# Optimization experiments

Measured on AMD Instinct MI355X. Metric: run time of the kernel, lower is better.

## Reference

```python
import jax, jax.numpy as jnp
import numpy as np

B, L, D, N, KEEP, HID = 64, 256, 128, 8192, 64, 1024
IN_DIM = D + KEEP * D + 1  # q + packed subset keys + log_count


def setup_inputs() -> dict:
    key = jax.random.key(0)
    ks = jax.random.split(key, 7)
    q = jax.random.normal(ks[0], (N, D), jnp.float32)
    k = jax.random.normal(ks[1], (B, L, D), jnp.float32)
    batch_idx = jax.random.randint(ks[2], (N,), 0, B)
    mask = jax.random.randint(ks[3], (N, L), 0, 2).astype(bool)
    count = jax.random.randint(ks[4], (N,), 0, L)
    W1 = jax.random.normal(ks[5], (IN_DIM, HID), jnp.float32) / np.sqrt(IN_DIM).astype(np.float32)
    b1 = jnp.zeros((HID,), jnp.float32)
    W2 = jax.random.normal(ks[6], (HID, 1), jnp.float32) / np.sqrt(HID).astype(np.float32)
    b2 = jnp.zeros((1,), jnp.float32)
    return dict(q=q, k=k, batch_idx=batch_idx, mask=mask, count=count,
                W1=W1, b1=b1, W2=W2, b2=b2)


def _pack_subset_keys(k, batch_idx, mask):
    # chain_k: [N, L, D] gather of per-chain key blocks
    chain_k = k[batch_idx]
    pos = jnp.arange(L, dtype=jnp.float32)
    # score = L - pos for masked positions, 0 otherwise -> topk picks first KEEP masked positions
    scores = mask.astype(jnp.float32) * (jnp.float32(L) - pos)[None, :]
    top_scores, top_idx = jax.lax.top_k(scores, KEEP)
    picked = top_scores > 0
    sortable = jnp.where(picked, top_idx, L)  # sentinel L for unpicked
    sortable = jnp.sort(sortable, axis=1)     # restore ascending position order
    picked = sortable < L
    safe_idx = jnp.where(picked, sortable, 0)
    packed = jnp.take_along_axis(chain_k, safe_idx[:, :, None], axis=1)  # [N, KEEP, D]
    packed = packed * picked[:, :, None].astype(packed.dtype)
    return packed.reshape(N, KEEP * D)


def reference(q, k, batch_idx, mask, count, W1, b1, W2, b2):
    packed = _pack_subset_keys(k, batch_idx, mask)
    log_count = jnp.log1p(count.astype(q.dtype))[:, None]
    feat = jnp.concatenate([q, packed, log_count], axis=-1)  # [N, IN_DIM]
    h = jax.nn.gelu(feat @ W1 + b1, approximate=False)       # torch GELU = exact erf
    return (h @ W2 + b2).squeeze(-1)                          # [N]
```

## Files before the change

### kernel.cpp

```cpp
#include <hip/hip_runtime.h>
#include <math.h>

#define N_ROWS 8192
#define B_CH   64
#define L_SEQ  256
#define D_DIM  128
#define KEEP   64
#define HID    1024
#define KTOT   8320

#define KOFF   (N_ROWS * D_DIM)
#define ZOFF   (KOFF + B_CH * L_SEQ * D_DIM)
#define BUF_ELEMS (ZOFF + 128)

#define QK_BLOCKS   1537
#define W1T_BLOCKS  2080
#define PACK_BLOCKS 64
#define OUT_BLOCKS  32
#define PREP_GRID   (QK_BLOCKS + W1T_BLOCKS + PACK_BLOCKS + OUT_BLOCKS)

typedef unsigned short ushort_t;
typedef __attribute__((ext_vector_type(8))) short  short8;
typedef __attribute__((ext_vector_type(4))) float  float4v;


__device__ __forceinline__ ushort_t f2bf(float f) {
    union { float f; unsigned int u; } v; v.f = f;
    unsigned int u = v.u;
    unsigned int r = u + 0x7fffu + ((u >> 16) & 1u);
    return (ushort_t)(r >> 16);
}

__device__ __forceinline__ void glds16(const void* g, void* l) {
    __builtin_amdgcn_global_load_lds(
        (const __attribute__((address_space(1))) unsigned int*)g,
        (__attribute__((address_space(3))) unsigned int*)l,
        16, 0, 0);
}

__global__ void prep(const float* __restrict__ q, const float* __restrict__ k,
                     const float* __restrict__ W1, const int* __restrict__ mask,
                     const int* __restrict__ batch_idx, const int* __restrict__ count,
                     const float* __restrict__ b2,
                     ushort_t* __restrict__ buf, ushort_t* __restrict__ w1t,
                     int* __restrict__ srcLUT, float* __restrict__ logc,
                     float* __restrict__ out) {
    __shared__ __align__(16) char smem[34304];
    const int blk = blockIdx.x;
    const int t = threadIdx.x;

    if (blk < QK_BLOCKS) {
        int c = blk * 256 + t;
        if (c >= BUF_ELEMS / 8) return;
        int e = c * 8;
        float4 x0, x1;
        if (e < KOFF) {
            const float4* s = (const float4*)(q + e);
            x0 = s[0]; x1 = s[1];
        } else if (e < ZOFF) {
            const float4* s = (const float4*)(k + (e - KOFF));
            x0 = s[0]; x1 = s[1];
        } else {
            x0 = make_float4(0.f, 0.f, 0.f, 0.f);
            x1 = x0;
        }
        union { ushort_t s[8]; uint4 v; } o;
        o.s[0] = f2bf(x0.x); o.s[1] = f2bf(x0.y); o.s[2] = f2bf(x0.z); o.s[3] = f2bf(x0.w);
        o.s[4] = f2bf(x1.x); o.s[5] = f2bf(x1.y); o.s[6] = f2bf(x1.z); o.s[7] = f2bf(x1.w);
        *(uint4*)(buf + e) = o.v;

    } else if (blk < QK_BLOCKS + W1T_BLOCKS) {
        const int idx = blk - QK_BLOCKS;
        const int k0 = (idx % 130) * 64, h0 = (idx / 130) * 64;
        float (*tile)[65] = (float(*)[65])smem;
        const int hl = t & 63, kl = t >> 6;
#pragma unroll
        for (int i = 0; i < 16; ++i) {
            int kk = kl + i * 4;
            tile[kk][hl] = W1[(size_t)(k0 + kk) * HID + h0 + hl];
        }
        __syncthreads();
#pragma unroll
        for (int i = 0; i < 2; ++i) {
            int chunk = i * 256 + t;
            int h = chunk >> 3, piece = chunk & 7;
            union { ushort_t s[8]; uint4 v; } o;
#pragma unroll
            for (int j = 0; j < 8; ++j) o.s[j] = f2bf(tile[piece * 8 + j][h]);
            *(uint4*)(w1t + (size_t)(h0 + h) * KTOT + k0 + piece * 8) = o.v;
        }

    } else if (blk < QK_BLOCKS + W1T_BLOCKS + PACK_BLOCKS) {
        const int p = blk - (QK_BLOCKS + W1T_BLOCKS);
        const int n0 = p * 128;
        int* sidx = (int*)smem;
        int* bidx_l = (int*)(smem + 33280);
        for (int i = t; i < 128 * 65; i += 256) sidx[i] = -1;
        if (t < 128) {
            int n = n0 + t;
            bidx_l[t] = batch_idx[n];
            logc[n] = log1pf((float)count[n]);
            srcLUT[n] = n * D_DIM;
        }
        __syncthreads();
        const int w = t >> 6, l = t & 63;
        const unsigned long long ltm = (1ull << l) - 1ull;
        for (int r = 0; r < 32; ++r) {
            const int lr = w * 32 + r;
            const int n = n0 + lr;
            const int* mrow = mask + (size_t)n * L_SEQ;
            int m0 = mrow[l] != 0;
            int m1 = mrow[64 + l] != 0;
            int m2 = mrow[128 + l] != 0;
            int m3 = mrow[192 + l] != 0;
            unsigned long long b0 = __ballot(m0), b1 = __ballot(m1);
            unsigned long long b2v = __ballot(m2), b3 = __ballot(m3);
            int p1 = (int)__popcll(b0);
            int p2 = p1 + (int)__popcll(b1);
            int p3 = p2 + (int)__popcll(b2v);
            int* row = sidx + lr * 65;
            if (m0) { int rk = (int)__popcll(b0 & ltm);      if (rk < KEEP) row[rk] = l; }
            if (m1) { int rk = p1 + (int)__popcll(b1 & ltm); if (rk < KEEP) row[rk] = 64 + l; }
            if (m2) { int rk = p2 + (int)__popcll(b2v & ltm); if (rk < KEEP) row[rk] = 128 + l; }
            if (m3) { int rk = p3 + (int)__popcll(b3 & ltm); if (rk < KEEP) row[rk] = 192 + l; }
        }
        __syncthreads();
        for (int e = t; e < KEEP * 128; e += 256) {
            int j = e >> 7, nl = e & 127;
            int s = sidx[nl * 65 + j];
            srcLUT[(size_t)(j + 1) * N_ROWS + n0 + nl] =
                (s >= 0) ? (KOFF + (bidx_l[nl] * L_SEQ + s) * D_DIM) : ZOFF;
        }

    } else {
        int i = (blk - (QK_BLOCKS + W1T_BLOCKS + PACK_BLOCKS)) * 256 + t;
        if (i < N_ROWS) out[i] = b2[0];
    }
}

__global__ __launch_bounds__(256, 2)
void gemm_mlp(const ushort_t* __restrict__ buf, const ushort_t* __restrict__ w1t,
              const int* __restrict__ srcLUT, const float* __restrict__ logc,
              const float* __restrict__ W1, const float* __restrict__ b1,
              const float* __restrict__ W2, float* __restrict__ out) {
    __shared__ ushort_t As[128 * 128];
    __shared__ ushort_t Bs[128 * 128];

    const int t = threadIdx.x;
    const int blkH = blockIdx.x, blkM = blockIdx.y;
    const int wave = t >> 6, lane = t & 63;
    const int wm = wave >> 1, wh = wave & 1;
    const int ln = lane & 15, quad = lane >> 4;

    float4v acc[4][4];
#pragma unroll
    for (int i = 0; i < 4; ++i)
#pragma unroll
        for (int j = 0; j < 4; ++j)
#pragma unroll
            for (int r = 0; r < 4; ++r) acc[i][j][r] = 0.0f;

    const int tr = t >> 4;
    const int slot = t & 15;
    const int pg = slot ^ tr;
    ushort_t* lA = As + t * 8;
    ushort_t* lB = Bs + t * 8;
    const ushort_t* gB[8];
#pragma unroll
    for (int i = 0; i < 8; ++i)
        gB[i] = w1t + (size_t)(blkH * 128 + i * 16 + tr) * KTOT + pg * 8;
    const int* lutBase = srcLUT + blkM * 128 + tr;

    int offA[8];
#pragma unroll
    for (int i = 0; i < 8; ++i) offA[i] = lutBase[i * 16];

    for (int bi = 0; bi < 65; ++bi) {
#pragma unroll
        for (int i = 0; i < 8; ++i) {
            glds16(buf + offA[i] + pg * 8, lA + i * 2048);
            glds16(gB[i] + bi * 128, lB + i * 2048);
        }
        int offN[8];
        if (bi < 64) {
#pragma unroll
            for (int i = 0; i < 8; ++i) offN[i] = lutBase[(bi + 1) * N_ROWS + i * 16];
        }
        __syncthreads();
#pragma unroll
        for (int kk = 0; kk < 4; ++kk) {
            short8 af[4], bfr[4];
#pragma unroll
            for (int mi = 0; mi < 4; ++mi) {
                const int row = wm * 64 + mi * 16 + ln;
                const int sl = (kk * 4 + quad) ^ ln;
                af[mi] = *(const short8*)(As + row * 128 + sl * 8);
            }
#pragma unroll
            for (int ni = 0; ni < 4; ++ni) {
                const int row = wh * 64 + ni * 16 + ln;
                const int sl = (kk * 4 + quad) ^ ln;
                bfr[ni] = *(const short8*)(Bs + row * 128 + sl * 8);
            }
#pragma unroll
            for (int mi = 0; mi < 4; ++mi)
#pragma unroll
                for (int ni = 0; ni < 4; ++ni)
                    acc[mi][ni] = __builtin_amdgcn_mfma_f32_16x16x32_bf16(
                        af[mi], bfr[ni], acc[mi][ni], 0, 0, 0);
        }
        __syncthreads();
#pragma unroll
        for (int i = 0; i < 8; ++i) offA[i] = offN[i];
    }

    const float* w1last = W1 + (size_t)KTOT * HID;
    float w1l[4], b1v[4], w2v[4];
#pragma unroll
    for (int ni = 0; ni < 4; ++ni) {
        int h = blkH * 128 + wh * 64 + ni * 16 + ln;
        w1l[ni] = w1last[h];
        b1v[ni] = b1[h];
        w2v[ni] = W2[h];
    }
    const int nbase = blkM * 128 + wm * 64 + quad * 4;
#pragma unroll
    for (int mi = 0; mi < 4; ++mi) {
#pragma unroll
        for (int rg = 0; rg < 4; ++rg) {
            const int n = nbase + mi * 16 + rg;
            const float lc = logc[n];
            float s = 0.0f;
#pragma unroll
            for (int ni = 0; ni < 4; ++ni) {
                float pre = acc[mi][ni][rg] + lc * w1l[ni] + b1v[ni];
                float hv = 0.5f * pre * (1.0f + erff(pre * 0.70710678118654752f));
                s += hv * w2v[ni];
            }
            s += __shfl_xor(s, 1);
            s += __shfl_xor(s, 2);
            s += __shfl_xor(s, 4);
            s += __shfl_xor(s, 8);
            if (ln == 0) atomicAdd(out + n, s);
        }
    }
}

extern "C" void kernel_launch(void* const* d_in, const int* in_sizes, int n_in,
                              void* d_out, int out_size, void* d_ws, size_t ws_size,
                              hipStream_t stream) {
    const float* q     = (const float*)d_in[0];
    const float* k     = (const float*)d_in[1];
    const int*   bidx  = (const int*)d_in[2];
    const int*   mask  = (const int*)d_in[3];
    const int*   count = (const int*)d_in[4];
    const float* W1    = (const float*)d_in[5];
    const float* b1    = (const float*)d_in[6];
    const float* W2    = (const float*)d_in[7];
    const float* b2    = (const float*)d_in[8];
    float* out = (float*)d_out;

    char* ws = (char*)d_ws;
    ushort_t* buf    = (ushort_t*)(ws);
    ushort_t* w1t    = (ushort_t*)(ws + 6291712);
    int*      srcLUT = (int*)(ws + 6291712 + 17039360);
    float*    logc   = (float*)(ws + 6291712 + 17039360 + 2129920);

    prep<<<PREP_GRID, 256, 0, stream>>>(q, k, W1, mask, bidx, count, b2,
                                        buf, w1t, srcLUT, logc, out);
    gemm_mlp<<<dim3(HID / 128, N_ROWS / 128), 256, 0, stream>>>(
        buf, w1t, srcLUT, logc, W1, b1, W2, out);
}
```

Before: 268.7 us.

## Double-buffer GEMM K-chunks in LDS and move finer-grained pack blocks first

The MLP GEMM now splits each 128-wide K block into two 64-wide chunks held in double-buffered LDS. The next chunk's global-to-LDS loads are issued before the MFMAs on the current chunk, leaving one barrier per chunk instead of two per block. LDS use per block also halves. In the prep kernel, mask packing uses 256 smaller blocks of 32 rows, scheduled first, so the serial ballot loop is shorter and overlaps with the conversion blocks. The cost is more loop iterations and some extra index bookkeeping for the LUT offsets across half-blocks.

```diff
diff --git a/kernel.cpp b/kernel.cpp
--- a/kernel.cpp
+++ b/kernel.cpp
@@ -13,16 +13,15 @@
 #define ZOFF   (KOFF + B_CH * L_SEQ * D_DIM)
 #define BUF_ELEMS (ZOFF + 128)
 
+#define PACK_BLOCKS 256
 #define QK_BLOCKS   1537
 #define W1T_BLOCKS  2080
-#define PACK_BLOCKS 64
 #define OUT_BLOCKS  32
-#define PREP_GRID   (QK_BLOCKS + W1T_BLOCKS + PACK_BLOCKS + OUT_BLOCKS)
+#define PREP_GRID   (PACK_BLOCKS + QK_BLOCKS + W1T_BLOCKS + OUT_BLOCKS)
 
 typedef unsigned short ushort_t;
 typedef __attribute__((ext_vector_type(8))) short  short8;
 typedef __attribute__((ext_vector_type(4))) float  float4v;
-
 
 __device__ __forceinline__ ushort_t f2bf(float f) {
     union { float f; unsigned int u; } v; v.f = f;
@@ -45,12 +44,52 @@
                      ushort_t* __restrict__ buf, ushort_t* __restrict__ w1t,
                      int* __restrict__ srcLUT, float* __restrict__ logc,
                      float* __restrict__ out) {
-    __shared__ __align__(16) char smem[34304];
+    __shared__ __align__(16) char smem[16640];
     const int blk = blockIdx.x;
     const int t = threadIdx.x;
 
-    if (blk < QK_BLOCKS) {
-        int c = blk * 256 + t;
+    if (blk < PACK_BLOCKS) {
+        const int n0 = blk * 32;
+        int* sidx = (int*)smem;
+        int* bidx_l = (int*)(smem + 32 * 65 * 4);
+        for (int i = t; i < 32 * 65; i += 256) sidx[i] = -1;
+        if (t < 32) {
+            int n = n0 + t;
+            bidx_l[t] = batch_idx[n];
+            logc[n] = log1pf((float)count[n]);
+            srcLUT[n] = n * D_DIM;
+        }
+        __syncthreads();
+        const int w = t >> 6, l = t & 63;
+        const unsigned long long ltm = (1ull << l) - 1ull;
+        for (int r = 0; r < 8; ++r) {
+            const int lr = w * 8 + r;
+            const int* mrow = mask + (size_t)(n0 + lr) * L_SEQ;
+            int m0 = mrow[l] != 0;
+            int m1 = mrow[64 + l] != 0;
+            int m2 = mrow[128 + l] != 0;
+            int m3 = mrow[192 + l] != 0;
+            unsigned long long b0 = __ballot(m0), b1 = __ballot(m1);
+            unsigned long long b2v = __ballot(m2), b3 = __ballot(m3);
+            int p1 = (int)__popcll(b0);
+            int p2 = p1 + (int)__popcll(b1);
+            int p3 = p2 + (int)__popcll(b2v);
+            int* row = sidx + lr * 65;
+            if (m0) { int rk = (int)__popcll(b0 & ltm);       if (rk < KEEP) row[rk] = l; }
+            if (m1) { int rk = p1 + (int)__popcll(b1 & ltm);  if (rk < KEEP) row[rk] = 64 + l; }
+            if (m2) { int rk = p2 + (int)__popcll(b2v & ltm); if (rk < KEEP) row[rk] = 128 + l; }
+            if (m3) { int rk = p3 + (int)__popcll(b3 & ltm);  if (rk < KEEP) row[rk] = 192 + l; }
+        }
+        __syncthreads();
+        for (int e = t; e < KEEP * 32; e += 256) {
+            int j = e >> 5, nl = e & 31;
+            int s = sidx[nl * 65 + j];
+            srcLUT[(size_t)(j + 1) * N_ROWS + n0 + nl] =
+                (s >= 0) ? (KOFF + (bidx_l[nl] * L_SEQ + s) * D_DIM) : ZOFF;
+        }
+
+    } else if (blk < PACK_BLOCKS + QK_BLOCKS) {
+        int c = (blk - PACK_BLOCKS) * 256 + t;
         if (c >= BUF_ELEMS / 8) return;
         int e = c * 8;
         float4 x0, x1;
@@ -69,8 +108,8 @@
         o.s[4] = f2bf(x1.x); o.s[5] = f2bf(x1.y); o.s[6] = f2bf(x1.z); o.s[7] = f2bf(x1.w);
         *(uint4*)(buf + e) = o.v;
 
-    } else if (blk < QK_BLOCKS + W1T_BLOCKS) {
-        const int idx = blk - QK_BLOCKS;
+    } else if (blk < PACK_BLOCKS + QK_BLOCKS + W1T_BLOCKS) {
+        const int idx = blk - (PACK_BLOCKS + QK_BLOCKS);
         const int k0 = (idx % 130) * 64, h0 = (idx / 130) * 64;
         float (*tile)[65] = (float(*)[65])smem;
         const int hl = t & 63, kl = t >> 6;
@@ -90,50 +129,8 @@
             *(uint4*)(w1t + (size_t)(h0 + h) * KTOT + k0 + piece * 8) = o.v;
         }
 
-    } else if (blk < QK_BLOCKS + W1T_BLOCKS + PACK_BLOCKS) {
-        const int p = blk - (QK_BLOCKS + W1T_BLOCKS);
-        const int n0 = p * 128;
-        int* sidx = (int*)smem;
-        int* bidx_l = (int*)(smem + 33280);
-        for (int i = t; i < 128 * 65; i += 256) sidx[i] = -1;
-        if (t < 128) {
-            int n = n0 + t;
-            bidx_l[t] = batch_idx[n];
-            logc[n] = log1pf((float)count[n]);
-            srcLUT[n] = n * D_DIM;
-        }
-        __syncthreads();
-        const int w = t >> 6, l = t & 63;
-        const unsigned long long ltm = (1ull << l) - 1ull;
-        for (int r = 0; r < 32; ++r) {
-            const int lr = w * 32 + r;
-            const int n = n0 + lr;
-            const int* mrow = mask + (size_t)n * L_SEQ;
-            int m0 = mrow[l] != 0;
-            int m1 = mrow[64 + l] != 0;
-            int m2 = mrow[128 + l] != 0;
-            int m3 = mrow[192 + l] != 0;
-            unsigned long long b0 = __ballot(m0), b1 = __ballot(m1);
-            unsigned long long b2v = __ballot(m2), b3 = __ballot(m3);
-            int p1 = (int)__popcll(b0);
-            int p2 = p1 + (int)__popcll(b1);
-            int p3 = p2 + (int)__popcll(b2v);
-            int* row = sidx + lr * 65;
-            if (m0) { int rk = (int)__popcll(b0 & ltm);      if (rk < KEEP) row[rk] = l; }
-            if (m1) { int rk = p1 + (int)__popcll(b1 & ltm); if (rk < KEEP) row[rk] = 64 + l; }
-            if (m2) { int rk = p2 + (int)__popcll(b2v & ltm); if (rk < KEEP) row[rk] = 128 + l; }
-            if (m3) { int rk = p3 + (int)__popcll(b3 & ltm); if (rk < KEEP) row[rk] = 192 + l; }
-        }
-        __syncthreads();
-        for (int e = t; e < KEEP * 128; e += 256) {
-            int j = e >> 7, nl = e & 127;
-            int s = sidx[nl * 65 + j];
-            srcLUT[(size_t)(j + 1) * N_ROWS + n0 + nl] =
-                (s >= 0) ? (KOFF + (bidx_l[nl] * L_SEQ + s) * D_DIM) : ZOFF;
-        }
-
     } else {
-        int i = (blk - (QK_BLOCKS + W1T_BLOCKS + PACK_BLOCKS)) * 256 + t;
+        int i = (blk - (PACK_BLOCKS + QK_BLOCKS + W1T_BLOCKS)) * 256 + t;
         if (i < N_ROWS) out[i] = b2[0];
     }
 }
@@ -143,8 +140,8 @@
               const int* __restrict__ srcLUT, const float* __restrict__ logc,
               const float* __restrict__ W1, const float* __restrict__ b1,
               const float* __restrict__ W2, float* __restrict__ out) {
-    __shared__ ushort_t As[128 * 128];
-    __shared__ ushort_t Bs[128 * 128];
+    __shared__ ushort_t As[2][128 * 64];
+    __shared__ ushort_t Bs[2][128 * 64];
 
     const int t = threadIdx.x;
     const int blkH = blockIdx.x, blkM = blockIdx.y;
@@ -160,47 +157,59 @@
 #pragma unroll
             for (int r = 0; r < 4; ++r) acc[i][j][r] = 0.0f;
 
-    const int tr = t >> 4;
-    const int slot = t & 15;
-    const int pg = slot ^ tr;
-    ushort_t* lA = As + t * 8;
-    ushort_t* lB = Bs + t * 8;
-    const ushort_t* gB[8];
-#pragma unroll
-    for (int i = 0; i < 8; ++i)
-        gB[i] = w1t + (size_t)(blkH * 128 + i * 16 + tr) * KTOT + pg * 8;
+    const int tr = t >> 3;
+    const int pg = (t & 7) ^ (tr & 7);
+    const ushort_t* gBp[4];
+#pragma unroll
+    for (int i = 0; i < 4; ++i)
+        gBp[i] = w1t + (size_t)(blkH * 128 + i * 32 + tr) * KTOT + pg * 8;
     const int* lutBase = srcLUT + blkM * 128 + tr;
 
-    int offA[8];
-#pragma unroll
-    for (int i = 0; i < 8; ++i) offA[i] = lutBase[i * 16];
-
-    for (int bi = 0; bi < 65; ++bi) {
-#pragma unroll
-        for (int i = 0; i < 8; ++i) {
-            glds16(buf + offA[i] + pg * 8, lA + i * 2048);
-            glds16(gB[i] + bi * 128, lB + i * 2048);
-        }
-        int offN[8];
-        if (bi < 64) {
-#pragma unroll
-            for (int i = 0; i < 8; ++i) offN[i] = lutBase[(bi + 1) * N_ROWS + i * 16];
-        }
-        __syncthreads();
-#pragma unroll
-        for (int kk = 0; kk < 4; ++kk) {
+    int offA[4], offN[4];
+#pragma unroll
+    for (int i = 0; i < 4; ++i) offA[i] = lutBase[i * 32];
+
+#pragma unroll
+    for (int i = 0; i < 4; ++i) {
+        glds16(buf + offA[i] + pg * 8, &As[0][(i * 256 + t) * 8]);
+        glds16(gBp[i], &Bs[0][(i * 256 + t) * 8]);
+    }
+
+    int p = 0;
+    for (int ch = 0; ch < 130; ++ch) {
+        __syncthreads();
+        const int nx = ch + 1;
+        if (nx < 130) {
+            const int half = nx & 1;
+            const int* offs = half ? offA : offN;
+            ushort_t* dA = &As[p ^ 1][0];
+            ushort_t* dB = &Bs[p ^ 1][0];
+#pragma unroll
+            for (int i = 0; i < 4; ++i) {
+                glds16(buf + offs[i] + half * 64 + pg * 8, dA + (i * 256 + t) * 8);
+                glds16(gBp[i] + nx * 64, dB + (i * 256 + t) * 8);
+            }
+        }
+        if ((ch & 1) == 0 && (ch >> 1) < 64) {
+#pragma unroll
+            for (int i = 0; i < 4; ++i) offN[i] = lutBase[((ch >> 1) + 1) * N_ROWS + i * 32];
+        }
+        const ushort_t* rA = &As[p][0];
+        const ushort_t* rB = &Bs[p][0];
+#pragma unroll
+        for (int kk = 0; kk < 2; ++kk) {
             short8 af[4], bfr[4];
 #pragma unroll
             for (int mi = 0; mi < 4; ++mi) {
                 const int row = wm * 64 + mi * 16 + ln;
-                const int sl = (kk * 4 + quad) ^ ln;
-                af[mi] = *(const short8*)(As + row * 128 + sl * 8);
+                const int sl = (kk * 4 + quad) ^ (ln & 7);
+                af[mi] = *(const short8*)(rA + row * 64 + sl * 8);
             }
 #pragma unroll
             for (int ni = 0; ni < 4; ++ni) {
                 const int row = wh * 64 + ni * 16 + ln;
-                const int sl = (kk * 4 + quad) ^ ln;
-                bfr[ni] = *(const short8*)(Bs + row * 128 + sl * 8);
+                const int sl = (kk * 4 + quad) ^ (ln & 7);
+                bfr[ni] = *(const short8*)(rB + row * 64 + sl * 8);
             }
 #pragma unroll
             for (int mi = 0; mi < 4; ++mi)
@@ -209,9 +218,11 @@
                     acc[mi][ni] = __builtin_amdgcn_mfma_f32_16x16x32_bf16(
                         af[mi], bfr[ni], acc[mi][ni], 0, 0, 0);
         }
-        __syncthreads();
-#pragma unroll
-        for (int i = 0; i < 8; ++i) offA[i] = offN[i];
+        if (ch & 1) {
+#pragma unroll
+            for (int i = 0; i < 4; ++i) offA[i] = offN[i];
+        }
+        p ^= 1;
     }
 
     const float* w1last = W1 + (size_t)KTOT * HID;
```

Result: faster. 255.6 us (-4.9%).

## Pre-swizzle W1 into MFMA fragment layout and load B directly to registers

Applied to the files above, without the earlier changes.

The W1 transpose in prep now writes bf16 weights in a per-lane MFMA fragment order, so the GEMM loads B operands straight from global memory into registers with coalesced 16-byte loads. This drops the B shared-memory tile, its global-to-LDS copies and its LDS reads, halving LDS use in the GEMM. The pack-subset work is split into more, smaller blocks placed first in the prep grid, and the output init is folded into them. The cost is higher register pressure from 16 short8 B fragments per iteration, and B loads that are no longer shared across the two M-waves.

```diff
diff --git a/kernel.cpp b/kernel.cpp
--- a/kernel.cpp
+++ b/kernel.cpp
@@ -8,21 +8,21 @@
 #define KEEP   64
 #define HID    1024
 #define KTOT   8320
+#define KTILES 260
+#define HTILES 64
 
 #define KOFF   (N_ROWS * D_DIM)
 #define ZOFF   (KOFF + B_CH * L_SEQ * D_DIM)
 #define BUF_ELEMS (ZOFF + 128)
 
+#define PACK_BLOCKS 256
 #define QK_BLOCKS   1537
 #define W1T_BLOCKS  2080
-#define PACK_BLOCKS 64
-#define OUT_BLOCKS  32
-#define PREP_GRID   (QK_BLOCKS + W1T_BLOCKS + PACK_BLOCKS + OUT_BLOCKS)
+#define PREP_GRID   (PACK_BLOCKS + QK_BLOCKS + W1T_BLOCKS)
 
 typedef unsigned short ushort_t;
 typedef __attribute__((ext_vector_type(8))) short  short8;
 typedef __attribute__((ext_vector_type(4))) float  float4v;
-
 
 __device__ __forceinline__ ushort_t f2bf(float f) {
     union { float f; unsigned int u; } v; v.f = f;
@@ -42,15 +42,56 @@
                      const float* __restrict__ W1, const int* __restrict__ mask,
                      const int* __restrict__ batch_idx, const int* __restrict__ count,
                      const float* __restrict__ b2,
-                     ushort_t* __restrict__ buf, ushort_t* __restrict__ w1t,
+                     ushort_t* __restrict__ buf, ushort_t* __restrict__ w1f,
                      int* __restrict__ srcLUT, float* __restrict__ logc,
                      float* __restrict__ out) {
-    __shared__ __align__(16) char smem[34304];
+    __shared__ __align__(16) char smem[16640];
     const int blk = blockIdx.x;
     const int t = threadIdx.x;
 
-    if (blk < QK_BLOCKS) {
-        int c = blk * 256 + t;
+    if (blk < PACK_BLOCKS) {
+        const int n0 = blk * 32;
+        int* sidx = (int*)smem;
+        int* bidx_l = (int*)(smem + 32 * 65 * 4);
+        for (int i = t; i < 32 * 65; i += 256) sidx[i] = -1;
+        if (t < 32) {
+            int n = n0 + t;
+            bidx_l[t] = batch_idx[n];
+            logc[n] = log1pf((float)count[n]);
+            srcLUT[n] = n * D_DIM;
+            out[n] = b2[0];
+        }
+        __syncthreads();
+        const int w = t >> 6, l = t & 63;
+        const unsigned long long ltm = (1ull << l) - 1ull;
+        for (int r = 0; r < 8; ++r) {
+            const int lr = w * 8 + r;
+            const int* mrow = mask + (size_t)(n0 + lr) * L_SEQ;
+            int m0 = mrow[l] != 0;
+            int m1 = mrow[64 + l] != 0;
+            int m2 = mrow[128 + l] != 0;
+            int m3 = mrow[192 + l] != 0;
+            unsigned long long b0 = __ballot(m0), b1 = __ballot(m1);
+            unsigned long long b2v = __ballot(m2), b3 = __ballot(m3);
+            int p1 = (int)__popcll(b0);
+            int p2 = p1 + (int)__popcll(b1);
+            int p3 = p2 + (int)__popcll(b2v);
+            int* row = sidx + lr * 65;
+            if (m0) { int rk = (int)__popcll(b0 & ltm);       if (rk < KEEP) row[rk] = l; }
+            if (m1) { int rk = p1 + (int)__popcll(b1 & ltm);  if (rk < KEEP) row[rk] = 64 + l; }
+            if (m2) { int rk = p2 + (int)__popcll(b2v & ltm); if (rk < KEEP) row[rk] = 128 + l; }
+            if (m3) { int rk = p3 + (int)__popcll(b3 & ltm);  if (rk < KEEP) row[rk] = 192 + l; }
+        }
+        __syncthreads();
+        for (int e = t; e < KEEP * 32; e += 256) {
+            int j = e >> 5, nl = e & 31;
+            int s = sidx[nl * 65 + j];
+            srcLUT[(size_t)(j + 1) * N_ROWS + n0 + nl] =
+                (s >= 0) ? (KOFF + (bidx_l[nl] * L_SEQ + s) * D_DIM) : ZOFF;
+        }
+
+    } else if (blk < PACK_BLOCKS + QK_BLOCKS) {
+        int c = (blk - PACK_BLOCKS) * 256 + t;
         if (c >= BUF_ELEMS / 8) return;
         int e = c * 8;
         float4 x0, x1;
@@ -69,8 +110,8 @@
         o.s[4] = f2bf(x1.x); o.s[5] = f2bf(x1.y); o.s[6] = f2bf(x1.z); o.s[7] = f2bf(x1.w);
         *(uint4*)(buf + e) = o.v;
 
-    } else if (blk < QK_BLOCKS + W1T_BLOCKS) {
-        const int idx = blk - QK_BLOCKS;
+    } else {
+        const int idx = blk - (PACK_BLOCKS + QK_BLOCKS);
         const int k0 = (idx % 130) * 64, h0 = (idx / 130) * 64;
         float (*tile)[65] = (float(*)[65])smem;
         const int hl = t & 63, kl = t >> 6;
@@ -82,69 +123,26 @@
         __syncthreads();
 #pragma unroll
         for (int i = 0; i < 2; ++i) {
-            int chunk = i * 256 + t;
-            int h = chunk >> 3, piece = chunk & 7;
-            union { ushort_t s[8]; uint4 v; } o;
-#pragma unroll
-            for (int j = 0; j < 8; ++j) o.s[j] = f2bf(tile[piece * 8 + j][h]);
-            *(uint4*)(w1t + (size_t)(h0 + h) * KTOT + k0 + piece * 8) = o.v;
-        }
-
-    } else if (blk < QK_BLOCKS + W1T_BLOCKS + PACK_BLOCKS) {
-        const int p = blk - (QK_BLOCKS + W1T_BLOCKS);
-        const int n0 = p * 128;
-        int* sidx = (int*)smem;
-        int* bidx_l = (int*)(smem + 33280);
-        for (int i = t; i < 128 * 65; i += 256) sidx[i] = -1;
-        if (t < 128) {
-            int n = n0 + t;
-            bidx_l[t] = batch_idx[n];
-            logc[n] = log1pf((float)count[n]);
-            srcLUT[n] = n * D_DIM;
-        }
-        __syncthreads();
-        const int w = t >> 6, l = t & 63;
-        const unsigned long long ltm = (1ull << l) - 1ull;
-        for (int r = 0; r < 32; ++r) {
-            const int lr = w * 32 + r;
-            const int n = n0 + lr;
-            const int* mrow = mask + (size_t)n * L_SEQ;
-            int m0 = mrow[l] != 0;
-            int m1 = mrow[64 + l] != 0;
-            int m2 = mrow[128 + l] != 0;
-            int m3 = mrow[192 + l] != 0;
-            unsigned long long b0 = __ballot(m0), b1 = __ballot(m1);
-            unsigned long long b2v = __ballot(m2), b3 = __ballot(m3);
-            int p1 = (int)__popcll(b0);
-            int p2 = p1 + (int)__popcll(b1);
-            int p3 = p2 + (int)__popcll(b2v);
-            int* row = sidx + lr * 65;
-            if (m0) { int rk = (int)__popcll(b0 & ltm);      if (rk < KEEP) row[rk] = l; }
-            if (m1) { int rk = p1 + (int)__popcll(b1 & ltm); if (rk < KEEP) row[rk] = 64 + l; }
-            if (m2) { int rk = p2 + (int)__popcll(b2v & ltm); if (rk < KEEP) row[rk] = 128 + l; }
-            if (m3) { int rk = p3 + (int)__popcll(b3 & ltm); if (rk < KEEP) row[rk] = 192 + l; }
-        }
-        __syncthreads();
-        for (int e = t; e < KEEP * 128; e += 256) {
-            int j = e >> 7, nl = e & 127;
-            int s = sidx[nl * 65 + j];
-            srcLUT[(size_t)(j + 1) * N_ROWS + n0 + nl] =
-                (s >= 0) ? (KOFF + (bidx_l[nl] * L_SEQ + s) * D_DIM) : ZOFF;
-        }
-
-    } else {
-        int i = (blk - (QK_BLOCKS + W1T_BLOCKS + PACK_BLOCKS)) * 256 + t;
-        if (i < N_ROWS) out[i] = b2[0];
+            int s = i * 256 + t;
+            int c = s >> 6, l = s & 63;
+            int qt = c >> 2, ht = c & 3;
+            int ln = l & 15, quad = l >> 4;
+            union { ushort_t sv[8]; uint4 v; } o;
+#pragma unroll
+            for (int j = 0; j < 8; ++j)
+                o.sv[j] = f2bf(tile[qt * 32 + quad * 8 + j][ht * 16 + ln]);
+            size_t dst = (((size_t)(h0 / 16 + ht) * KTILES + (k0 / 32 + qt)) * 64 + l) * 8;
+            *(uint4*)(w1f + dst) = o.v;
+        }
     }
 }
 
 __global__ __launch_bounds__(256, 2)
-void gemm_mlp(const ushort_t* __restrict__ buf, const ushort_t* __restrict__ w1t,
+void gemm_mlp(const ushort_t* __restrict__ buf, const ushort_t* __restrict__ w1f,
               const int* __restrict__ srcLUT, const float* __restrict__ logc,
               const float* __restrict__ W1, const float* __restrict__ b1,
               const float* __restrict__ W2, float* __restrict__ out) {
     __shared__ ushort_t As[128 * 128];
-    __shared__ ushort_t Bs[128 * 128];
 
     const int t = threadIdx.x;
     const int blkH = blockIdx.x, blkM = blockIdx.y;
@@ -161,26 +159,29 @@
             for (int r = 0; r < 4; ++r) acc[i][j][r] = 0.0f;
 
     const int tr = t >> 4;
-    const int slot = t & 15;
-    const int pg = slot ^ tr;
+    const int pg = (t & 15) ^ tr;
     ushort_t* lA = As + t * 8;
-    ushort_t* lB = Bs + t * 8;
-    const ushort_t* gB[8];
-#pragma unroll
-    for (int i = 0; i < 8; ++i)
-        gB[i] = w1t + (size_t)(blkH * 128 + i * 16 + tr) * KTOT + pg * 8;
     const int* lutBase = srcLUT + blkM * 128 + tr;
 
+    const ushort_t* bp[4];
+#pragma unroll
+    for (int ni = 0; ni < 4; ++ni)
+        bp[ni] = w1f + ((size_t)(blkH * 8 + wh * 4 + ni) * KTILES * 64 + lane) * 8;
+
     int offA[8];
 #pragma unroll
     for (int i = 0; i < 8; ++i) offA[i] = lutBase[i * 16];
 
     for (int bi = 0; bi < 65; ++bi) {
 #pragma unroll
-        for (int i = 0; i < 8; ++i) {
+        for (int i = 0; i < 8; ++i)
             glds16(buf + offA[i] + pg * 8, lA + i * 2048);
-            glds16(gB[i] + bi * 128, lB + i * 2048);
-        }
+        short8 bq[4][4];
+#pragma unroll
+        for (int kk = 0; kk < 4; ++kk)
+#pragma unroll
+            for (int ni = 0; ni < 4; ++ni)
+                bq[kk][ni] = *(const short8*)(bp[ni] + (size_t)(bi * 4 + kk) * 512);
         int offN[8];
         if (bi < 64) {
 #pragma unroll
@@ -189,7 +190,7 @@
         __syncthreads();
 #pragma unroll
         for (int kk = 0; kk < 4; ++kk) {
-            short8 af[4], bfr[4];
+            short8 af[4];
 #pragma unroll
             for (int mi = 0; mi < 4; ++mi) {
                 const int row = wm * 64 + mi * 16 + ln;
@@ -197,17 +198,11 @@
                 af[mi] = *(const short8*)(As + row * 128 + sl * 8);
             }
 #pragma unroll
-            for (int ni = 0; ni < 4; ++ni) {
-                const int row = wh * 64 + ni * 16 + ln;
-                const int sl = (kk * 4 + quad) ^ ln;
-                bfr[ni] = *(const short8*)(Bs + row * 128 + sl * 8);
-            }
-#pragma unroll
             for (int mi = 0; mi < 4; ++mi)
 #pragma unroll
                 for (int ni = 0; ni < 4; ++ni)
                     acc[mi][ni] = __builtin_amdgcn_mfma_f32_16x16x32_bf16(
-                        af[mi], bfr[ni], acc[mi][ni], 0, 0, 0);
+                        af[mi], bq[kk][ni], acc[mi][ni], 0, 0, 0);
         }
         __syncthreads();
 #pragma unroll
@@ -262,12 +257,12 @@
 
     char* ws = (char*)d_ws;
     ushort_t* buf    = (ushort_t*)(ws);
-    ushort_t* w1t    = (ushort_t*)(ws + 6291712);
+    ushort_t* w1f    = (ushort_t*)(ws + 6291712);
     int*      srcLUT = (int*)(ws + 6291712 + 17039360);
     float*    logc   = (float*)(ws + 6291712 + 17039360 + 2129920);
 
     prep<<<PREP_GRID, 256, 0, stream>>>(q, k, W1, mask, bidx, count, b2,
-                                        buf, w1t, srcLUT, logc, out);
+                                        buf, w1f, srcLUT, logc, out);
     gemm_mlp<<<dim3(HID / 128, N_ROWS / 128), 256, 0, stream>>>(
-        buf, w1t, srcLUT, logc, W1, b1, W2, out);
-}
+        buf, w1f, srcLUT, logc, W1, b1, W2, out);
+}
```

Result: faster. 243.0 us (-9.6%).
